# Optimization experiments

Measured on AMD Instinct MI355X. Metric: run time of the kernel, lower is better.

The kernel has to match this reference:

```python
import jax, jax.numpy as jnp
import numpy as np


def _closest_distance_sum(p1, p2):
    # p1: [B, N, 3], p2: [B, M, 3]
    # squared Euclidean distance of each p1 point to nearest p2 point, summed.
    # d2[b,n,m] = |p1[b,n]|^2 + |p2[b,m]|^2 - 2 <p1[b,n], p2[b,m]>
    sq1 = jnp.sum(p1 * p1, axis=-1)                      # [B, N]
    sq2 = jnp.sum(p2 * p2, axis=-1)                      # [B, M]
    cross = jnp.einsum('bnd,bmd->bnm', p1, p2)           # [B, N, M]
    d2 = sq1[:, :, None] + sq2[:, None, :] - 2.0 * cross
    d2 = jnp.maximum(d2, 0.0)  # numerical floor (true sq-dist is >= 0)
    return jnp.sum(jnp.min(d2, axis=2))


def setup_inputs() -> dict:
    key = jax.random.key(0)
    k1, k2 = jax.random.split(key)
    shape_xyz = jax.random.normal(k1, (4, 8192, 3), dtype=jnp.float32)
    skel_xyz = jax.random.normal(k2, (4, 2048, 3), dtype=jnp.float32)
    return {"shape_xyz": shape_xyz, "skel_xyz": skel_xyz}


def reference(shape_xyz, skel_xyz):
    cd1 = _closest_distance_sum(shape_xyz, skel_xyz)
    cd2 = _closest_distance_sum(skel_xyz, shape_xyz)
    loss_cd = (cd1 + cd2) * 0.0001
    return loss_cd
```

## Files before the change

kernel.cpp:

```cpp
#include <hip/hip_runtime.h>


#define QPT    16
#define BIGF   3.4e38f

#define P2_OFF   1048576
#define PSUM_OFF 2097152
#define RBLOCKS  640

#define PAIR(J)                                                            \
    {                                                                      \
        float4 ta = lds[lbase + (J) + 0];                                  \
        float4 tb = lds[lbase + (J) + 1];                                  \
        _Pragma("unroll")                                                  \
        for (int k = 0; k < QPT; ++k) {                                    \
            float e0 = fmaf(nqx[k], ta.x,                                  \
                       fmaf(nqy[k], ta.y, fmaf(nqz[k], ta.z, ta.w)));      \
            float e1 = fmaf(nqx[k], tb.x,                                  \
                       fmaf(nqy[k], tb.y, fmaf(nqz[k], tb.z, tb.w)));      \
            mn[k] = fminf(fminf(mn[k], e0), e1);                           \
        }                                                                  \
    }

__global__ __launch_bounds__(256) void chamfer_kernel(
    const float* __restrict__ shape,
    const float* __restrict__ skel,
    float* __restrict__ pw)
{
    const int b   = blockIdx.y;
    const int tid = threadIdx.x;

    const float* q; float* pbase; const float* ssrc;
    int q0, qstride, lbase, scount;
    int x = blockIdx.x;
    if (x < 64) {
        const int qb = x >> 5, ch = x & 31;
        pbase   = pw + ((size_t)b * 32 + ch) * 8192;
        q0      = qb * 4096 + tid;
        qstride = 256;
        lbase   = 0;  scount = 64;
        ssrc    = skel + ((size_t)b * 2048 + ch * 64) * 3;
        q       = shape + (size_t)b * 8192 * 3;
    } else {
        const int z = x - 64, half = tid >> 7;
        const int ch = 2 * z + half;
        pbase   = pw + P2_OFF + ((size_t)b * 128 + ch) * 2048;
        q0      = tid & 127;
        qstride = 128;
        lbase   = half * 64;  scount = 128;
        ssrc    = shape + ((size_t)b * 8192 + z * 128) * 3;
        q       = skel + (size_t)b * 2048 * 3;
    }

    __shared__ float4 lds[128];

    if (tid < scount) {
        float tx = ssrc[tid * 3 + 0], ty = ssrc[tid * 3 + 1], tz = ssrc[tid * 3 + 2];
        lds[tid] = make_float4(tx, ty, tz, tx * tx + ty * ty + tz * tz);
    }

    const float* qp = q + (size_t)q0 * 3;
    const int qs3 = qstride * 3;
    float nqx[QPT], nqy[QPT], nqz[QPT], qsq[QPT], mn[QPT];
    #pragma unroll
    for (int k = 0; k < QPT; ++k) {
        float xq = qp[k * qs3 + 0];
        float yq = qp[k * qs3 + 1];
        float zq = qp[k * qs3 + 2];
        nqx[k] = -2.0f * xq; nqy[k] = -2.0f * yq; nqz[k] = -2.0f * zq;
        qsq[k] = xq * xq + yq * yq + zq * zq;
        mn[k]  = BIGF;
    }

    __syncthreads();

    const int P = ((tid >> 6) & 3) * 8;
    #pragma unroll 1
    for (int j = 0; j < P; j += 2)
        PAIR(j);

    #pragma unroll 2
    for (int j = P; j < 64; j += 2)
        PAIR(j);

    #pragma unroll
    for (int k = 0; k < QPT; ++k)
        pbase[q0 + k * qstride] = qsq[k] + mn[k];
}

__global__ __launch_bounds__(256) void reduce_kernel(
    const float* __restrict__ pw, float* __restrict__ psum)
{
    const int blk = blockIdx.x, tid = threadIdx.x;
    const int sub = tid & 3, qi = tid >> 2;

    float m = BIGF;
    if (blk < 512) {
        const int b  = blk >> 7;
        const int ql = ((blk & 127) << 6) + qi;
        const float* p = pw + (size_t)b * 32 * 8192 + ql;
        #pragma unroll
        for (int i = 0; i < 8; ++i)
            m = fminf(m, p[(sub * 8 + i) * 8192]);
    } else {
        const int z  = blk - 512;
        const int b  = z >> 5;
        const int ql = ((z & 31) << 6) + qi;
        const float* p = pw + P2_OFF + (size_t)b * 128 * 2048 + ql;
        #pragma unroll
        for (int i = 0; i < 32; ++i)
            m = fminf(m, p[(sub * 32 + i) * 2048]);
    }

    m = fminf(m, __shfl_xor(m, 1));
    m = fminf(m, __shfl_xor(m, 2));
    float s = (sub == 0) ? fmaxf(m, 0.0f) : 0.0f;

    #pragma unroll
    for (int off = 32; off > 0; off >>= 1)
        s += __shfl_down(s, off);

    __shared__ float wsum[4];
    const int lane = tid & 63, w = tid >> 6;
    if (lane == 0) wsum[w] = s;
    __syncthreads();
    if (tid == 0) psum[blk] = (wsum[0] + wsum[1]) + (wsum[2] + wsum[3]);
}

__global__ __launch_bounds__(256) void final_kernel(
    const float* __restrict__ psum, float* __restrict__ out)
{
    float s = psum[threadIdx.x] + psum[threadIdx.x + 256];
    if (threadIdx.x < 128) s += psum[threadIdx.x + 512];

    #pragma unroll
    for (int off = 32; off > 0; off >>= 1)
        s += __shfl_down(s, off);

    __shared__ float wsum[4];
    const int lane = threadIdx.x & 63, w = threadIdx.x >> 6;
    if (lane == 0) wsum[w] = s;
    __syncthreads();
    if (threadIdx.x == 0)
        out[0] = ((wsum[0] + wsum[1]) + (wsum[2] + wsum[3])) * 1.0e-4f;
}

extern "C" void kernel_launch(void* const* d_in, const int* in_sizes, int n_in,
                              void* d_out, int out_size, void* d_ws, size_t ws_size,
                              hipStream_t stream) {
    const float* shape = (const float*)d_in[0];
    const float* skel  = (const float*)d_in[1];
    float* out         = (float*)d_out;
    float* pw          = (float*)d_ws;

    chamfer_kernel<<<dim3(128, 4), 256, 0, stream>>>(shape, skel, pw);

    reduce_kernel<<<RBLOCKS, 256, 0, stream>>>(pw, pw + PSUM_OFF);
    final_kernel<<<1, 256, 0, stream>>>(pw + PSUM_OFF, out);
}
```

Before: 24.84 us.

## Rotate target points across wave lanes with DPP instead of LDS broadcast

Each lane now holds one of 64 target points in registers. Wave-wide DPP rotate-by-one moves (wave_ror) cycle every target through every lane over 32 iterations of two points each. This removes the shared-memory staging, the __syncthreads, and the per-iteration LDS reads, along with the staggered start offsets that were there to avoid LDS conflicts. In exchange it adds eight DPP moves per pair of targets and relies on wave-level DPP rotation being supported on this architecture.

New measurement: 29.78 us. 1.2x slower.

```diff
diff --git a/kernel.cpp b/kernel.cpp
--- a/kernel.cpp
+++ b/kernel.cpp
@@ -8,37 +8,28 @@
 #define PSUM_OFF 2097152
 #define RBLOCKS  640
 
-#define PAIR(J)                                                            \
-    {                                                                      \
-        float4 ta = lds[lbase + (J) + 0];                                  \
-        float4 tb = lds[lbase + (J) + 1];                                  \
-        _Pragma("unroll")                                                  \
-        for (int k = 0; k < QPT; ++k) {                                    \
-            float e0 = fmaf(nqx[k], ta.x,                                  \
-                       fmaf(nqy[k], ta.y, fmaf(nqz[k], ta.z, ta.w)));      \
-            float e1 = fmaf(nqx[k], tb.x,                                  \
-                       fmaf(nqy[k], tb.y, fmaf(nqz[k], tb.z, tb.w)));      \
-            mn[k] = fminf(fminf(mn[k], e0), e1);                           \
-        }                                                                  \
-    }
+__device__ __forceinline__ float ror1(float v) {
+    return __int_as_float(__builtin_amdgcn_update_dpp(
+        0, __float_as_int(v), 0x13C, 0xF, 0xF, true));
+}
 
 __global__ __launch_bounds__(256) void chamfer_kernel(
     const float* __restrict__ shape,
     const float* __restrict__ skel,
     float* __restrict__ pw)
 {
-    const int b   = blockIdx.y;
-    const int tid = threadIdx.x;
+    const int b    = blockIdx.y;
+    const int tid  = threadIdx.x;
+    const int lane = tid & 63;
 
     const float* q; float* pbase; const float* ssrc;
-    int q0, qstride, lbase, scount;
+    int q0, qstride;
     int x = blockIdx.x;
     if (x < 64) {
         const int qb = x >> 5, ch = x & 31;
         pbase   = pw + ((size_t)b * 32 + ch) * 8192;
         q0      = qb * 4096 + tid;
         qstride = 256;
-        lbase   = 0;  scount = 64;
         ssrc    = skel + ((size_t)b * 2048 + ch * 64) * 3;
         q       = shape + (size_t)b * 8192 * 3;
     } else {
@@ -47,17 +38,14 @@
         pbase   = pw + P2_OFF + ((size_t)b * 128 + ch) * 2048;
         q0      = tid & 127;
         qstride = 128;
-        lbase   = half * 64;  scount = 128;
-        ssrc    = shape + ((size_t)b * 8192 + z * 128) * 3;
+        ssrc    = shape + ((size_t)b * 8192 + z * 128 + half * 64) * 3;
         q       = skel + (size_t)b * 2048 * 3;
     }
 
-    __shared__ float4 lds[128];
-
-    if (tid < scount) {
-        float tx = ssrc[tid * 3 + 0], ty = ssrc[tid * 3 + 1], tz = ssrc[tid * 3 + 2];
-        lds[tid] = make_float4(tx, ty, tz, tx * tx + ty * ty + tz * tz);
-    }
+    float tx = ssrc[lane * 3 + 0];
+    float ty = ssrc[lane * 3 + 1];
+    float tz = ssrc[lane * 3 + 2];
+    float tw = fmaf(tx, tx, fmaf(ty, ty, tz * tz));
 
     const float* qp = q + (size_t)q0 * 3;
     const int qs3 = qstride * 3;
@@ -72,16 +60,19 @@
         mn[k]  = BIGF;
     }
 
-    __syncthreads();
-
-    const int P = ((tid >> 6) & 3) * 8;
-    #pragma unroll 1
-    for (int j = 0; j < P; j += 2)
-        PAIR(j);
-
-    #pragma unroll 2
-    for (int j = P; j < 64; j += 2)
-        PAIR(j);
+    #pragma unroll 4
+    for (int j = 0; j < 32; ++j) {
+        float bx = ror1(tx), by = ror1(ty), bz = ror1(tz), bw = ror1(tw);
+        #pragma unroll
+        for (int k = 0; k < QPT; ++k) {
+            float e0 = fmaf(nqx[k], tx,
+                       fmaf(nqy[k], ty, fmaf(nqz[k], tz, tw)));
+            float e1 = fmaf(nqx[k], bx,
+                       fmaf(nqy[k], by, fmaf(nqz[k], bz, bw)));
+            mn[k] = fminf(fminf(mn[k], e0), e1);
+        }
+        tx = ror1(bx); ty = ror1(by); tz = ror1(bz); tw = ror1(bw);
+    }
 
     #pragma unroll
     for (int k = 0; k < QPT; ++k)
```
